# Kernel tuning notes

Measured on AMD Instinct MI355X. Metric: run time of the kernel, lower is better.

## Reference

```python
import jax, jax.numpy as jnp
import numpy as np
from jax import lax

N = 100000   # num_nodes
E = 1600000  # num_edges (avg degree 16)
F = 128      # num_features
H = 256      # hidden_channels
C = 64       # num_classes
K = 10       # propagation steps
ALPHA = 0.1
BETA = 0.5
THETA = 0.5
EPS = 1e-5   # BatchNorm eps


def setup_inputs() -> dict:
    key = jax.random.key(0)
    ks = jax.random.split(key, 16)
    x = jax.random.normal(ks[0], (N, F), dtype=jnp.float32)
    src = jax.random.randint(ks[1], (E,), 0, N, dtype=jnp.int32)
    dst = jax.random.randint(ks[2], (E,), 0, N, dtype=jnp.int32)
    # row-normalized adjacency weights so repeated A@z stays bounded
    deg = jax.ops.segment_sum(jnp.ones((E,), jnp.float32), dst, num_segments=N)
    w = (1.0 / jnp.maximum(deg, 1.0))[dst]
    # MLP params (Linear + BatchNorm per hidden layer)
    W1 = jax.random.normal(ks[3], (F, H), dtype=jnp.float32) * 0.05
    b1 = jnp.zeros((H,), jnp.float32)
    g1 = jnp.ones((H,), jnp.float32)
    be1 = jnp.zeros((H,), jnp.float32)
    W2 = jax.random.normal(ks[4], (H, H), dtype=jnp.float32) * 0.05
    b2 = jnp.zeros((H,), jnp.float32)
    g2 = jnp.ones((H,), jnp.float32)
    be2 = jnp.zeros((H,), jnp.float32)
    W3 = jax.random.normal(ks[5], (H, C), dtype=jnp.float32) * 0.05
    b3 = jnp.zeros((C,), jnp.float32)
    # lazy caches (warm-start memories); nonzero so the blend branch is taken
    z_sam = jax.random.normal(ks[6], (N, C), dtype=jnp.float32) * 0.1
    g_sam = jax.random.normal(ks[7], (N, C), dtype=jnp.float32) * 0.01
    return dict(x=x, src=src, dst=dst, w=w,
                W1=W1, b1=b1, g1=g1, be1=be1,
                W2=W2, b2=b2, g2=g2, be2=be2,
                W3=W3, b3=b3, z_sam=z_sam, g_sam=g_sam, size=N)


def _bn(h, gamma, beta):
    # BatchNorm1d in training mode: batch statistics over nodes
    mu = jnp.mean(h, axis=0)
    var = jnp.var(h, axis=0)
    return (h - mu) * jax.lax.rsqrt(var + EPS) * gamma + beta


def reference(x, src, dst, w, W1, b1, g1, be1, W2, b2, g2, be2, W3, b3,
              z_sam, g_sam, size):
    # MLP stack: Linear -> BN -> ReLU (dropout omitted: deterministic reference)
    h = jax.nn.relu(_bn(x @ W1 + b1, g1, be1))
    h = jax.nn.relu(_bn(h @ W2 + b2, g2, be2))
    logits = h @ W3 + b3  # [N, C]

    def spmm(z):
        # (A @ z)_i = sum_{j -> i} w_ij * z_j
        return jax.ops.segment_sum(z[src] * w[:, None], dst, num_segments=N)

    # Lazy_Prop.forward: warm-start blend, then K propagation steps
    use_x = jnp.all(z_sam[:size] == 0.0)
    z0 = jnp.where(use_x, logits, (1.0 - BETA) * z_sam + BETA * logits)
    z = lax.fori_loop(0, K, lambda i, z: (1.0 - ALPHA) * spmm(z) + ALPHA * logits, z0)
    return jax.nn.log_softmax(z, axis=1)
```

## Files before the change

kernel.cpp:

```cpp
#include <hip/hip_runtime.h>
#include <hip/hip_bf16.h>

#define NODES 100000
#define EDGES 1600000
#define FEAT  128
#define HID   256
#define CLS   64
#define KPROP 10
#define ALPHA_C 0.1f
#define BETA_C  0.5f
#define BN_EPS  1e-5f

typedef __attribute__((ext_vector_type(8))) short short8;
typedef __attribute__((ext_vector_type(4))) float f32x4;

static __device__ __forceinline__ unsigned short f2b(float f) {
    __hip_bfloat16 h = __float2bfloat16(f);
    return *(unsigned short*)&h;
}
static __device__ __forceinline__ float b2f(unsigned short u) {
    __hip_bfloat16 h;
    *(unsigned short*)&h = u;
    return __bfloat162float(h);
}
static __device__ __forceinline__ float asf(unsigned int u) {
    union { unsigned int u; float f; } c; c.u = u; return c.f;
}

__global__ void packwt_k(const float* __restrict__ W, unsigned short* __restrict__ Wt,
                         int K, int N)
{
    int i = blockIdx.x * 256 + threadIdx.x;
    if (i < K * N) {
        int k = i / N, n = i - k * N;
        Wt[(size_t)n * K + k] = f2b(W[i]);
    }
}

template<bool AF32, bool FUSE, bool STATS, bool OUTF32, int KK, int NCOLG>
__global__ __launch_bounds__(256, 2)
void gemm_lds_k(const void* __restrict__ Ain, const unsigned short* __restrict__ Wt,
                const float* __restrict__ bias,
                const float* __restrict__ scale, const float* __restrict__ shift,
                void* __restrict__ outp,
                float* __restrict__ gsum, float* __restrict__ gsq,
                int M, int N, int nchunks, int nblk)
{
    constexpr int NK8 = KK / 32;
    __shared__ unsigned short Blds[64 * KK];
    __shared__ float Slds[KK];
    __shared__ float Hlds[KK];

    const int lane = threadIdx.x & 63;
    const int wv   = threadIdx.x >> 6;
    const int quad = lane >> 4;
    const int l16  = lane & 15;
    const int colg = (NCOLG > 1) ? (blockIdx.x % NCOLG) : 0;
    const int blk0 = (NCOLG > 1) ? (blockIdx.x / NCOLG) : blockIdx.x;
    const int colbase = colg * 64;

    {
        const unsigned short* wp = Wt + (size_t)colbase * KK;
        constexpr int ELEMS = 64 * KK / 8;
        #pragma unroll
        for (int i0 = 0; i0 < ELEMS; i0 += 256) {
            int i  = i0 + threadIdx.x;
            int c  = i / (KK / 8);
            int k8 = i - c * (KK / 8);
            short8 v = *(const short8*)(wp + (size_t)c * KK + k8 * 8);
            int byte = c * (KK * 2) + ((k8 * 16) ^ ((c & 7) << 4));
            *(short8*)((char*)Blds + byte) = v;
        }
        if constexpr (FUSE) {
            for (int i = threadIdx.x; i < KK; i += 256) {
                Slds[i] = scale[i];
                Hlds[i] = shift[i];
            }
        }
    }
    __syncthreads();

    float bcol[4];
    #pragma unroll
    for (int ct = 0; ct < 4; ++ct) bcol[ct] = bias[colbase + ct * 16 + l16];

    float ps[4] = {0.f, 0.f, 0.f, 0.f};
    float pq[4] = {0.f, 0.f, 0.f, 0.f};

    float4 af0[2][AF32 ? NK8 : 1][2];
    float4 af1[2][AF32 ? NK8 : 1][2];
    short8 ah0[2][AF32 ? 1 : NK8];
    short8 ah1[2][AF32 ? 1 : NK8];

#define LOAD_A(AF, AH, CHK)                                                    \
    if ((CHK) < nchunks) {                                                     \
        const int rb_ = (CHK) * 128 + wv * 32;                                 \
        _Pragma("unroll")                                                      \
        for (int rt = 0; rt < 2; ++rt) {                                       \
            const int row_ = rb_ + rt * 16 + l16;                              \
            const bool ok_ = row_ < M;                                         \
            if constexpr (AF32) {                                              \
                const float* ap_ = (const float*)Ain + (size_t)row_ * KK + quad * 8; \
                _Pragma("unroll")                                              \
                for (int ks = 0; ks < NK8; ++ks) {                             \
                    AF[rt][ks][0] = ok_ ? *(const float4*)(ap_ + ks * 32)                \
                                        : (float4){0.f, 0.f, 0.f, 0.f};        \
                    AF[rt][ks][1] = ok_ ? *(const float4*)(ap_ + ks * 32 + 4)            \
                                        : (float4){0.f, 0.f, 0.f, 0.f};        \
                }                                                              \
            } else {                                                           \
                const unsigned short* ap_ = (const unsigned short*)Ain + (size_t)row_ * KK + quad * 8; \
                _Pragma("unroll")                                              \
                for (int ks = 0; ks < NK8; ++ks)                               \
                    AH[rt][ks] = ok_ ? *(const short8*)(ap_ + ks * 32)         \
                                     : (short8){0, 0, 0, 0, 0, 0, 0, 0};       \
            }                                                                  \
        }                                                                      \
    }

#define COMPUTE(AF, AH, CHK)                                                   \
    {                                                                          \
        const int rb_ = (CHK) * 128 + wv * 32;                                 \
        f32x4 acc[2][4];                                                       \
        _Pragma("unroll")                                                      \
        for (int i = 0; i < 2; ++i)                                            \
            _Pragma("unroll")                                                  \
            for (int j = 0; j < 4; ++j)                                        \
                acc[i][j] = (f32x4){0.f, 0.f, 0.f, 0.f};                       \
        _Pragma("unroll")                                                      \
        for (int ks = 0; ks < NK8; ++ks) {                                     \
            const int k_ = ks * 32 + quad * 8;                                 \
            float sc[8], sh[8];                                                \
            if constexpr (FUSE) {                                              \
                float4 s0 = *(const float4*)&Slds[k_];                         \
                float4 s1 = *(const float4*)&Slds[k_ + 4];                     \
                float4 h0 = *(const float4*)&Hlds[k_];                         \
                float4 h1 = *(const float4*)&Hlds[k_ + 4];                     \
                sc[0]=s0.x; sc[1]=s0.y; sc[2]=s0.z; sc[3]=s0.w;                \
                sc[4]=s1.x; sc[5]=s1.y; sc[6]=s1.z; sc[7]=s1.w;                \
                sh[0]=h0.x; sh[1]=h0.y; sh[2]=h0.z; sh[3]=h0.w;                \
                sh[4]=h1.x; sh[5]=h1.y; sh[6]=h1.z; sh[7]=h1.w;                \
            }                                                                  \
            short8 a2[2];                                                      \
            _Pragma("unroll")                                                  \
            for (int rt = 0; rt < 2; ++rt) {                                   \
                float v[8];                                                    \
                if constexpr (AF32) {                                          \
                    float4 t0 = AF[rt][ks][0];                                 \
                    float4 t1 = AF[rt][ks][1];                                 \
                    v[0]=t0.x; v[1]=t0.y; v[2]=t0.z; v[3]=t0.w;                \
                    v[4]=t1.x; v[5]=t1.y; v[6]=t1.z; v[7]=t1.w;                \
                } else {                                                       \
                    _Pragma("unroll")                                          \
                    for (int j = 0; j < 8; ++j)                                \
                        v[j] = b2f((unsigned short)AH[rt][ks][j]);             \
                }                                                              \
                if constexpr (FUSE) {                                          \
                    _Pragma("unroll")                                          \
                    for (int j = 0; j < 8; ++j)                                \
                        v[j] = fmaxf(fmaf(v[j], sc[j], sh[j]), 0.f);           \
                }                                                              \
                short8 av;                                                     \
                _Pragma("unroll")                                              \
                for (int j = 0; j < 8; ++j) av[j] = (short)f2b(v[j]);          \
                a2[rt] = av;                                                   \
            }                                                                  \
            _Pragma("unroll")                                                  \
            for (int ct = 0; ct < 4; ++ct) {                                   \
                const int boff = (ct * 16 + l16) * (KK * 2)                    \
                               + ((ks * 64 + quad * 16) ^ ((l16 & 7) << 4));   \
                short8 bf = *(const short8*)((const char*)Blds + boff);        \
                acc[0][ct] = __builtin_amdgcn_mfma_f32_16x16x32_bf16(a2[0], bf, acc[0][ct], 0, 0, 0); \
                acc[1][ct] = __builtin_amdgcn_mfma_f32_16x16x32_bf16(a2[1], bf, acc[1][ct], 0, 0, 0); \
            }                                                                  \
        }                                                                      \
        _Pragma("unroll")                                                      \
        for (int ct = 0; ct < 4; ++ct) {                                       \
            const int col_ = colbase + ct * 16 + l16;                          \
            _Pragma("unroll")                                                  \
            for (int rt = 0; rt < 2; ++rt) {                                   \
                _Pragma("unroll")                                              \
                for (int r2 = 0; r2 < 4; ++r2) {                               \
                    const int row_ = rb_ + rt * 16 + quad * 4 + r2;            \
                    if (row_ < M) {                                            \
                        float vv = acc[rt][ct][r2] + bcol[ct];                 \
                        if constexpr (STATS) { ps[ct] += vv; pq[ct] += vv * vv; } \
                        if constexpr (OUTF32) {                                \
                            ((float*)outp)[(size_t)row_ * N + col_] = vv;      \
                        } else {                                               \
                            ((unsigned short*)outp)[(size_t)row_ * N + col_] = f2b(vv); \
                        }                                                      \
                    }                                                          \
                }                                                              \
            }                                                                  \
        }                                                                      \
    }

    int chunk = blk0;
    LOAD_A(af0, ah0, chunk)
    while (chunk < nchunks) {
        const int cn1 = chunk + nblk;
        LOAD_A(af1, ah1, cn1)
        __builtin_amdgcn_sched_barrier(0);
        COMPUTE(af0, ah0, chunk)
        chunk = cn1;
        if (chunk >= nchunks) break;
        const int cn2 = chunk + nblk;
        LOAD_A(af0, ah0, cn2)
        __builtin_amdgcn_sched_barrier(0);
        COMPUTE(af1, ah1, chunk)
        chunk = cn2;
    }
#undef LOAD_A
#undef COMPUTE

    if constexpr (STATS) {
        #pragma unroll
        for (int ct = 0; ct < 4; ++ct) {
            float s = ps[ct];
            s += __shfl_xor(s, 16, 64);
            s += __shfl_xor(s, 32, 64);
            float q = pq[ct];
            q += __shfl_xor(q, 16, 64);
            q += __shfl_xor(q, 32, 64);
            if (lane < 16) {
                atomicAdd(&gsum[colbase + ct * 16 + lane], s);
                atomicAdd(&gsq[colbase + ct * 16 + lane], q);
            }
        }
    }
}

__global__ void bnfin_k(const float* __restrict__ sum, const float* __restrict__ sq,
                        const float* __restrict__ g, const float* __restrict__ be,
                        float* __restrict__ scale, float* __restrict__ shift)
{
    int c = threadIdx.x;
    float mu = sum[c] * (1.f / NODES);
    float var = sq[c] * (1.f / NODES) - mu * mu;
    float sc = g[c] * rsqrtf(var + BN_EPS);
    scale[c] = sc;
    shift[c] = be[c] - mu * sc;
}

__global__ void flag_k(const float* __restrict__ zs, int* __restrict__ flag)
{
    int i = blockIdx.x * 256 + threadIdx.x;
    bool nz = (i < NODES * CLS) && (zs[i] != 0.f);
    if (__any(nz)) {
        if ((threadIdx.x & 63) == 0) *flag = 1;
    }
}

__global__ void blend_k(const float* __restrict__ zs, const float* __restrict__ logits,
                        const int* __restrict__ flag, unsigned short* __restrict__ z0)
{
    int i = blockIdx.x * 256 + threadIdx.x;
    if (i < NODES * CLS) {
        float l = logits[i];
        float v = (*flag) ? ((1.f - BETA_C) * zs[i] + BETA_C * l) : l;
        z0[i] = f2b(v);
    }
}

__global__ void count_k(const int* __restrict__ dst, int* __restrict__ cntx)
{
    int t = blockIdx.x * 256 + threadIdx.x;
    if (t >= EDGES / 4) return;
    int4 d = ((const int4*)dst)[t];
    int* c = cntx + (size_t)(blockIdx.x & 7) * NODES;
    atomicAdd(&c[d.x], 1);
    atomicAdd(&c[d.y], 1);
    atomicAdd(&c[d.z], 1);
    atomicAdd(&c[d.w], 1);
}

__global__ void sumoff_k(int* __restrict__ cntx, int* __restrict__ cnt)
{
    int n = blockIdx.x * 256 + threadIdx.x;
    if (n >= NODES) return;
    int tot = 0;
    int p[8];
    #pragma unroll
    for (int x = 0; x < 8; ++x) {
        p[x] = tot;
        tot += cntx[(size_t)x * NODES + n];
    }
    #pragma unroll
    for (int x = 0; x < 8; ++x)
        cntx[(size_t)x * NODES + n] = p[x];
    cnt[n] = tot;
}

__global__ void scan1_k(const int* __restrict__ cnt, int* __restrict__ rowptr,
                        int* __restrict__ bsum)
{
    __shared__ int s[256];
    int tid = threadIdx.x;
    int i = blockIdx.x * 256 + tid;
    int v = (i < NODES) ? cnt[i] : 0;
    s[tid] = v;
    __syncthreads();
    for (int off = 1; off < 256; off <<= 1) {
        int t = (tid >= off) ? s[tid - off] : 0;
        __syncthreads();
        s[tid] += t;
        __syncthreads();
    }
    if (i < NODES) rowptr[i] = s[tid] - v;
    if (tid == 255) bsum[blockIdx.x] = s[255];
}

__global__ void scan2_k(const int* __restrict__ bsum, int* __restrict__ boffs, int nb)
{
    __shared__ int s[512];
    int tid = threadIdx.x;
    int v = (tid < nb) ? bsum[tid] : 0;
    s[tid] = v;
    __syncthreads();
    for (int off = 1; off < 512; off <<= 1) {
        int t = (tid >= off) ? s[tid - off] : 0;
        __syncthreads();
        s[tid] += t;
        __syncthreads();
    }
    if (tid < nb) boffs[tid] = s[tid] - v;
}

__global__ void scan3_k(int* __restrict__ rowptr, const int* __restrict__ boffs,
                        const int* __restrict__ cntx, int* __restrict__ curx)
{
    int i = blockIdx.x * 256 + threadIdx.x;
    if (i < NODES) {
        int v = rowptr[i] + boffs[blockIdx.x];
        rowptr[i] = v;
        #pragma unroll
        for (int x = 0; x < 8; ++x)
            curx[(size_t)x * NODES + i] = v + cntx[(size_t)x * NODES + i];
    }
    if (i == 0) rowptr[NODES] = EDGES;
}

__global__ void fill_k(const int* __restrict__ src, const int* __restrict__ dst,
                       int* __restrict__ curx, int* __restrict__ esrc)
{
    int t = blockIdx.x * 256 + threadIdx.x;
    if (t >= EDGES / 4) return;
    int4 d = ((const int4*)dst)[t];
    int4 s = ((const int4*)src)[t];
    int* cur = curx + (size_t)(blockIdx.x & 7) * NODES;
    int p0 = atomicAdd(&cur[d.x], 1);
    int p1 = atomicAdd(&cur[d.y], 1);
    int p2 = atomicAdd(&cur[d.z], 1);
    int p3 = atomicAdd(&cur[d.w], 1);
    esrc[p0] = s.x;
    esrc[p1] = s.y;
    esrc[p2] = s.z;
    esrc[p3] = s.w;
}

__global__ __launch_bounds__(256)
void prop_k(const int* __restrict__ rowptr, const int* __restrict__ esrc,
            const unsigned long long* __restrict__ zin, const float* __restrict__ logits,
            unsigned long long* __restrict__ zout)
{
    int row = blockIdx.x * 16 + (threadIdx.x >> 4);
    if (row >= NODES) return;
    int l16 = threadIdx.x & 15;
    int beg = rowptr[row], end = rowptr[row + 1];
    float a0 = 0.f, a1 = 0.f, a2 = 0.f, a3 = 0.f;

    for (int cbeg = beg; cbeg < end; cbeg += 16) {
        int e = cbeg + l16;
        int s_l = (e < end) ? esrc[e] : 0;
        int cnt = min(16, end - cbeg);
        if (cnt == 16) {
            int idx[16];
            #pragma unroll
            for (int u = 0; u < 16; ++u) idx[u] = __shfl(s_l, u, 16);
            unsigned long long vv[16];
            #pragma unroll
            for (int u = 0; u < 16; ++u)
                vv[u] = __hip_atomic_load(zin + (size_t)idx[u] * 16 + l16,
                                          __ATOMIC_RELAXED, __HIP_MEMORY_SCOPE_AGENT);
            #pragma unroll
            for (int u = 0; u < 16; ++u) {
                unsigned int lo = (unsigned int)vv[u];
                unsigned int hi = (unsigned int)(vv[u] >> 32);
                a0 += asf(lo << 16);
                a1 += asf(lo & 0xffff0000u);
                a2 += asf(hi << 16);
                a3 += asf(hi & 0xffff0000u);
            }
        } else {
            int j = 0;
            for (; j + 8 <= cnt; j += 8) {
                int idx[8];
                #pragma unroll
                for (int u = 0; u < 8; ++u) idx[u] = __shfl(s_l, j + u, 16);
                unsigned long long vv[8];
                #pragma unroll
                for (int u = 0; u < 8; ++u)
                    vv[u] = __hip_atomic_load(zin + (size_t)idx[u] * 16 + l16,
                                              __ATOMIC_RELAXED, __HIP_MEMORY_SCOPE_AGENT);
                #pragma unroll
                for (int u = 0; u < 8; ++u) {
                    unsigned int lo = (unsigned int)vv[u];
                    unsigned int hi = (unsigned int)(vv[u] >> 32);
                    a0 += asf(lo << 16);
                    a1 += asf(lo & 0xffff0000u);
                    a2 += asf(hi << 16);
                    a3 += asf(hi & 0xffff0000u);
                }
            }
            for (; j < cnt; ++j) {
                int s0 = __shfl(s_l, j, 16);
                unsigned long long v = __hip_atomic_load(zin + (size_t)s0 * 16 + l16,
                                                         __ATOMIC_RELAXED, __HIP_MEMORY_SCOPE_AGENT);
                unsigned int lo = (unsigned int)v;
                unsigned int hi = (unsigned int)(v >> 32);
                a0 += asf(lo << 16);
                a1 += asf(lo & 0xffff0000u);
                a2 += asf(hi << 16);
                a3 += asf(hi & 0xffff0000u);
            }
        }
    }
    float dg = (float)(end - beg);
    float inv = 1.f / fmaxf(dg, 1.f);
    float4 lv = *(const float4*)(logits + (size_t)row * CLS + l16 * 4);
    float cc = (1.f - ALPHA_C) * inv;
    float r0 = cc * a0 + ALPHA_C * lv.x;
    float r1 = cc * a1 + ALPHA_C * lv.y;
    float r2 = cc * a2 + ALPHA_C * lv.z;
    float r3 = cc * a3 + ALPHA_C * lv.w;
    unsigned int w0 = ((unsigned int)f2b(r1) << 16) | (unsigned int)f2b(r0);
    unsigned int w1 = ((unsigned int)f2b(r3) << 16) | (unsigned int)f2b(r2);
    zout[(size_t)row * 16 + l16] = ((unsigned long long)w1 << 32) | w0;
}

__global__ __launch_bounds__(256)
void logsoftmax_k(const unsigned short* __restrict__ z, float* __restrict__ out)
{
    int row = blockIdx.x * 4 + (threadIdx.x >> 6);
    if (row >= NODES) return;
    int lane = threadIdx.x & 63;
    float v = b2f(z[(size_t)row * CLS + lane]);
    float m = v;
    #pragma unroll
    for (int off = 32; off > 0; off >>= 1) m = fmaxf(m, __shfl_xor(m, off, 64));
    float ex = expf(v - m);
    float s = ex;
    #pragma unroll
    for (int off = 32; off > 0; off >>= 1) s += __shfl_xor(s, off, 64);
    out[(size_t)row * CLS + lane] = (v - m) - logf(s);
}

extern "C" void kernel_launch(void* const* d_in, const int* in_sizes, int n_in,
                              void* d_out, int out_size, void* d_ws, size_t ws_size,
                              hipStream_t stream)
{
    const float* x   = (const float*)d_in[0];
    const int*   src = (const int*)d_in[1];
    const int*   dst = (const int*)d_in[2];
    const float* W1  = (const float*)d_in[4];
    const float* b1  = (const float*)d_in[5];
    const float* g1  = (const float*)d_in[6];
    const float* be1 = (const float*)d_in[7];
    const float* W2  = (const float*)d_in[8];
    const float* b2  = (const float*)d_in[9];
    const float* g2  = (const float*)d_in[10];
    const float* be2 = (const float*)d_in[11];
    const float* W3  = (const float*)d_in[12];
    const float* b3  = (const float*)d_in[13];
    const float* zsam = (const float*)d_in[14];
    float* outp = (float*)d_out;

    uint8_t* base = (uint8_t*)d_ws;
    float* s_scale1 = (float*)(base);
    float* s_shift1 = s_scale1 + 256;
    float* s_scale2 = s_shift1 + 256;
    float* s_shift2 = s_scale2 + 256;
    float* s_sum    = s_shift2 + 256;
    float* s_sq     = s_sum + 256;
    int*   flag     = (int*)(s_sq + 256);

    unsigned short* Wt1 = (unsigned short*)(base + (1 << 14));
    unsigned short* Wt2 = Wt1 + (size_t)FEAT * HID;
    unsigned short* Wt3 = Wt2 + (size_t)HID * HID;
    unsigned short* h1  = Wt3 + (size_t)HID * CLS;
    unsigned short* h2  = h1 + (size_t)NODES * HID;
    float* logits = (float*)(h2 + (size_t)NODES * HID);
    unsigned short* zA  = (unsigned short*)(logits + (size_t)NODES * CLS);
    unsigned short* zB  = zA + (size_t)NODES * CLS;
    int* esrc   = (int*)(zB + (size_t)NODES * CLS);
    int* cntx   = esrc + EDGES;
    int* curx   = cntx + (size_t)8 * NODES;
    int* rowptr = curx + (size_t)8 * NODES;
    int* cnt    = rowptr + (NODES + 1);
    int* bsum   = cnt + NODES;
    int* boffs  = bsum + 512;

    const int NCHUNK = (NODES + 127) / 128;
    const int NBLK   = (NCHUNK + 1) / 2;
    const int SCANB  = (NODES + 255) / 256;
    const int EB4    = (EDGES / 4 + 255) / 256;

    packwt_k<<<(FEAT * HID + 255) / 256, 256, 0, stream>>>(W1, Wt1, FEAT, HID);
    packwt_k<<<(HID * HID + 255) / 256, 256, 0, stream>>>(W2, Wt2, HID, HID);
    packwt_k<<<(HID * CLS + 255) / 256, 256, 0, stream>>>(W3, Wt3, HID, CLS);

    hipMemsetAsync(cntx, 0, (size_t)8 * NODES * sizeof(int), stream);
    count_k<<<EB4, 256, 0, stream>>>(dst, cntx);
    sumoff_k<<<SCANB, 256, 0, stream>>>(cntx, cnt);
    scan1_k<<<SCANB, 256, 0, stream>>>(cnt, rowptr, bsum);
    scan2_k<<<1, 512, 0, stream>>>(bsum, boffs, SCANB);
    scan3_k<<<SCANB, 256, 0, stream>>>(rowptr, boffs, cntx, curx);
    fill_k<<<EB4, 256, 0, stream>>>(src, dst, curx, esrc);

    hipMemsetAsync(s_sum, 0, 512 * sizeof(float), stream);
    gemm_lds_k<true, false, true, false, FEAT, 4><<<NBLK * 4, 256, 0, stream>>>(
        x, Wt1, b1, nullptr, nullptr, h1, s_sum, s_sq, NODES, HID, NCHUNK, NBLK);
    bnfin_k<<<1, 256, 0, stream>>>(s_sum, s_sq, g1, be1, s_scale1, s_shift1);

    hipMemsetAsync(s_sum, 0, 512 * sizeof(float), stream);
    gemm_lds_k<false, true, true, false, HID, 4><<<NBLK * 4, 256, 0, stream>>>(
        h1, Wt2, b2, s_scale1, s_shift1, h2, s_sum, s_sq, NODES, HID, NCHUNK, NBLK);
    bnfin_k<<<1, 256, 0, stream>>>(s_sum, s_sq, g2, be2, s_scale2, s_shift2);

    gemm_lds_k<false, true, false, true, HID, 1><<<NBLK, 256, 0, stream>>>(
        h2, Wt3, b3, s_scale2, s_shift2, logits, nullptr, nullptr, NODES, CLS, NCHUNK, NBLK);

    hipMemsetAsync(flag, 0, sizeof(int), stream);
    flag_k<<<(NODES * CLS + 255) / 256, 256, 0, stream>>>(zsam, flag);
    blend_k<<<(NODES * CLS + 255) / 256, 256, 0, stream>>>(zsam, logits, flag, zA);

    const int PROPB = (NODES + 15) / 16;
    for (int it = 0; it < KPROP; ++it) {
        const unsigned long long* zi = (const unsigned long long*)((it & 1) ? zB : zA);
        unsigned long long* zo = (unsigned long long*)((it & 1) ? zA : zB);
        prop_k<<<PROPB, 256, 0, stream>>>(rowptr, esrc, zi, logits, zo);
    }

    logsoftmax_k<<<(NODES + 3) / 4, 256, 0, stream>>>(zA, outp);
}
```

Baseline: 905.7 us.

## Use 8 lanes per row with 16-byte gathers in prop; split CSR fill

```diff
diff --git a/kernel.cpp b/kernel.cpp
--- a/kernel.cpp
+++ b/kernel.cpp
@@ -341,102 +341,106 @@
     if (i == 0) rowptr[NODES] = EDGES;
 }
 
-__global__ void fill_k(const int* __restrict__ src, const int* __restrict__ dst,
-                       int* __restrict__ curx, int* __restrict__ esrc)
+__global__ void posfill_k(const int* __restrict__ dst, int* __restrict__ curx,
+                          int* __restrict__ pos)
 {
     int t = blockIdx.x * 256 + threadIdx.x;
     if (t >= EDGES / 4) return;
     int4 d = ((const int4*)dst)[t];
-    int4 s = ((const int4*)src)[t];
     int* cur = curx + (size_t)(blockIdx.x & 7) * NODES;
-    int p0 = atomicAdd(&cur[d.x], 1);
-    int p1 = atomicAdd(&cur[d.y], 1);
-    int p2 = atomicAdd(&cur[d.z], 1);
-    int p3 = atomicAdd(&cur[d.w], 1);
-    esrc[p0] = s.x;
-    esrc[p1] = s.y;
-    esrc[p2] = s.z;
-    esrc[p3] = s.w;
+    int4 p;
+    p.x = atomicAdd(&cur[d.x], 1);
+    p.y = atomicAdd(&cur[d.y], 1);
+    p.z = atomicAdd(&cur[d.z], 1);
+    p.w = atomicAdd(&cur[d.w], 1);
+    ((int4*)pos)[t] = p;
+}
+
+__global__ void scat_k(const int* __restrict__ src, const int* __restrict__ pos,
+                       int* __restrict__ esrc)
+{
+    int e = blockIdx.x * 256 + threadIdx.x;
+    if (e < EDGES) esrc[pos[e]] = src[e];
 }
 
 __global__ __launch_bounds__(256)
 void prop_k(const int* __restrict__ rowptr, const int* __restrict__ esrc,
             const unsigned long long* __restrict__ zin, const float* __restrict__ logits,
-            unsigned long long* __restrict__ zout)
-{
-    int row = blockIdx.x * 16 + (threadIdx.x >> 4);
+            uint4* __restrict__ zout)
+{
+    int row = blockIdx.x * 32 + (threadIdx.x >> 3);
     if (row >= NODES) return;
-    int l16 = threadIdx.x & 15;
+    int l8 = threadIdx.x & 7;
     int beg = rowptr[row], end = rowptr[row + 1];
     float a0 = 0.f, a1 = 0.f, a2 = 0.f, a3 = 0.f;
+    float a4 = 0.f, a5 = 0.f, a6 = 0.f, a7 = 0.f;
 
     for (int cbeg = beg; cbeg < end; cbeg += 16) {
-        int e = cbeg + l16;
-        int s_l = (e < end) ? esrc[e] : 0;
+        int e0 = cbeg + l8, e1 = cbeg + 8 + l8;
+        int s0 = (e0 < end) ? esrc[e0] : 0;
+        int s1 = (e1 < end) ? esrc[e1] : 0;
         int cnt = min(16, end - cbeg);
         if (cnt == 16) {
             int idx[16];
             #pragma unroll
-            for (int u = 0; u < 16; ++u) idx[u] = __shfl(s_l, u, 16);
-            unsigned long long vv[16];
+            for (int u = 0; u < 8; ++u) idx[u] = __shfl(s0, u, 8);
             #pragma unroll
-            for (int u = 0; u < 16; ++u)
-                vv[u] = __hip_atomic_load(zin + (size_t)idx[u] * 16 + l16,
-                                          __ATOMIC_RELAXED, __HIP_MEMORY_SCOPE_AGENT);
+            for (int u = 0; u < 8; ++u) idx[8 + u] = __shfl(s1, u, 8);
+            unsigned long long vv[32];
             #pragma unroll
             for (int u = 0; u < 16; ++u) {
-                unsigned int lo = (unsigned int)vv[u];
-                unsigned int hi = (unsigned int)(vv[u] >> 32);
-                a0 += asf(lo << 16);
-                a1 += asf(lo & 0xffff0000u);
-                a2 += asf(hi << 16);
-                a3 += asf(hi & 0xffff0000u);
+                const unsigned long long* p = zin + (size_t)idx[u] * 16 + l8 * 2;
+                vv[2 * u]     = __hip_atomic_load(p,     __ATOMIC_RELAXED, __HIP_MEMORY_SCOPE_AGENT);
+                vv[2 * u + 1] = __hip_atomic_load(p + 1, __ATOMIC_RELAXED, __HIP_MEMORY_SCOPE_AGENT);
+            }
+            #pragma unroll
+            for (int u = 0; u < 16; ++u) {
+                unsigned int x0 = (unsigned int)vv[2 * u];
+                unsigned int x1 = (unsigned int)(vv[2 * u] >> 32);
+                unsigned int x2 = (unsigned int)vv[2 * u + 1];
+                unsigned int x3 = (unsigned int)(vv[2 * u + 1] >> 32);
+                a0 += asf(x0 << 16);  a1 += asf(x0 & 0xffff0000u);
+                a2 += asf(x1 << 16);  a3 += asf(x1 & 0xffff0000u);
+                a4 += asf(x2 << 16);  a5 += asf(x2 & 0xffff0000u);
+                a6 += asf(x3 << 16);  a7 += asf(x3 & 0xffff0000u);
             }
         } else {
-            int j = 0;
-            for (; j + 8 <= cnt; j += 8) {
-                int idx[8];
-                #pragma unroll
-                for (int u = 0; u < 8; ++u) idx[u] = __shfl(s_l, j + u, 16);
-                unsigned long long vv[8];
-                #pragma unroll
-                for (int u = 0; u < 8; ++u)
-                    vv[u] = __hip_atomic_load(zin + (size_t)idx[u] * 16 + l16,
-                                              __ATOMIC_RELAXED, __HIP_MEMORY_SCOPE_AGENT);
-                #pragma unroll
-                for (int u = 0; u < 8; ++u) {
-                    unsigned int lo = (unsigned int)vv[u];
-                    unsigned int hi = (unsigned int)(vv[u] >> 32);
-                    a0 += asf(lo << 16);
-                    a1 += asf(lo & 0xffff0000u);
-                    a2 += asf(hi << 16);
-                    a3 += asf(hi & 0xffff0000u);
-                }
-            }
-            for (; j < cnt; ++j) {
-                int s0 = __shfl(s_l, j, 16);
-                unsigned long long v = __hip_atomic_load(zin + (size_t)s0 * 16 + l16,
-                                                         __ATOMIC_RELAXED, __HIP_MEMORY_SCOPE_AGENT);
-                unsigned int lo = (unsigned int)v;
-                unsigned int hi = (unsigned int)(v >> 32);
-                a0 += asf(lo << 16);
-                a1 += asf(lo & 0xffff0000u);
-                a2 += asf(hi << 16);
-                a3 += asf(hi & 0xffff0000u);
+            for (int j = 0; j < cnt; ++j) {
+                int sv = (j < 8) ? __shfl(s0, j, 8) : __shfl(s1, j - 8, 8);
+                const unsigned long long* p = zin + (size_t)sv * 16 + l8 * 2;
+                unsigned long long v0 = __hip_atomic_load(p,     __ATOMIC_RELAXED, __HIP_MEMORY_SCOPE_AGENT);
+                unsigned long long v1 = __hip_atomic_load(p + 1, __ATOMIC_RELAXED, __HIP_MEMORY_SCOPE_AGENT);
+                unsigned int x0 = (unsigned int)v0;
+                unsigned int x1 = (unsigned int)(v0 >> 32);
+                unsigned int x2 = (unsigned int)v1;
+                unsigned int x3 = (unsigned int)(v1 >> 32);
+                a0 += asf(x0 << 16);  a1 += asf(x0 & 0xffff0000u);
+                a2 += asf(x1 << 16);  a3 += asf(x1 & 0xffff0000u);
+                a4 += asf(x2 << 16);  a5 += asf(x2 & 0xffff0000u);
+                a6 += asf(x3 << 16);  a7 += asf(x3 & 0xffff0000u);
             }
         }
     }
     float dg = (float)(end - beg);
     float inv = 1.f / fmaxf(dg, 1.f);
-    float4 lv = *(const float4*)(logits + (size_t)row * CLS + l16 * 4);
     float cc = (1.f - ALPHA_C) * inv;
-    float r0 = cc * a0 + ALPHA_C * lv.x;
-    float r1 = cc * a1 + ALPHA_C * lv.y;
-    float r2 = cc * a2 + ALPHA_C * lv.z;
-    float r3 = cc * a3 + ALPHA_C * lv.w;
-    unsigned int w0 = ((unsigned int)f2b(r1) << 16) | (unsigned int)f2b(r0);
-    unsigned int w1 = ((unsigned int)f2b(r3) << 16) | (unsigned int)f2b(r2);
-    zout[(size_t)row * 16 + l16] = ((unsigned long long)w1 << 32) | w0;
+    const float* lp = logits + (size_t)row * CLS + l8 * 8;
+    float4 lv0 = *(const float4*)lp;
+    float4 lv1 = *(const float4*)(lp + 4);
+    float r0 = cc * a0 + ALPHA_C * lv0.x;
+    float r1 = cc * a1 + ALPHA_C * lv0.y;
+    float r2 = cc * a2 + ALPHA_C * lv0.z;
+    float r3 = cc * a3 + ALPHA_C * lv0.w;
+    float r4 = cc * a4 + ALPHA_C * lv1.x;
+    float r5 = cc * a5 + ALPHA_C * lv1.y;
+    float r6 = cc * a6 + ALPHA_C * lv1.z;
+    float r7 = cc * a7 + ALPHA_C * lv1.w;
+    uint4 w;
+    w.x = ((unsigned int)f2b(r1) << 16) | (unsigned int)f2b(r0);
+    w.y = ((unsigned int)f2b(r3) << 16) | (unsigned int)f2b(r2);
+    w.z = ((unsigned int)f2b(r5) << 16) | (unsigned int)f2b(r4);
+    w.w = ((unsigned int)f2b(r7) << 16) | (unsigned int)f2b(r6);
+    zout[(size_t)row * 8 + l8] = w;
 }
 
 __global__ __launch_bounds__(256)
@@ -500,6 +504,7 @@
     int* cnt    = rowptr + (NODES + 1);
     int* bsum   = cnt + NODES;
     int* boffs  = bsum + 512;
+    int* pos    = (int*)h1;
 
     const int NCHUNK = (NODES + 127) / 128;
     const int NBLK   = (NCHUNK + 1) / 2;
@@ -516,7 +521,8 @@
     scan1_k<<<SCANB, 256, 0, stream>>>(cnt, rowptr, bsum);
     scan2_k<<<1, 512, 0, stream>>>(bsum, boffs, SCANB);
     scan3_k<<<SCANB, 256, 0, stream>>>(rowptr, boffs, cntx, curx);
-    fill_k<<<EB4, 256, 0, stream>>>(src, dst, curx, esrc);
+    posfill_k<<<EB4, 256, 0, stream>>>(dst, curx, pos);
+    scat_k<<<EDGES / 256, 256, 0, stream>>>(src, pos, esrc);
 
     hipMemsetAsync(s_sum, 0, 512 * sizeof(float), stream);
     gemm_lds_k<true, false, true, false, FEAT, 4><<<NBLK * 4, 256, 0, stream>>>(
@@ -535,10 +541,10 @@
     flag_k<<<(NODES * CLS + 255) / 256, 256, 0, stream>>>(zsam, flag);
     blend_k<<<(NODES * CLS + 255) / 256, 256, 0, stream>>>(zsam, logits, flag, zA);
 
-    const int PROPB = (NODES + 15) / 16;
+    const int PROPB = (NODES + 31) / 32;
     for (int it = 0; it < KPROP; ++it) {
         const unsigned long long* zi = (const unsigned long long*)((it & 1) ? zB : zA);
-        unsigned long long* zo = (unsigned long long*)((it & 1) ? zA : zB);
+        uint4* zo = (uint4*)((it & 1) ? zA : zB);
         prop_k<<<PROPB, 256, 0, stream>>>(rowptr, esrc, zi, logits, zo);
     }
 
```

After: 902.4 us. Within noise of the previous version (-0.4%).
